# Kernel tuning notes

Hardware: AMD Instinct MI355X
Metric: run time of the kernel (lower is better)

The kernel has to match this reference:

```python
import jax, jax.numpy as jnp
import numpy as np

TEMP = 0.05
STRENGTH = 0.5

def setup_inputs() -> dict:
    key = jax.random.key(0)
    features = jax.random.normal(key, (8, 48, 48, 768), dtype=jnp.float32)
    return {"features": features}

def reference(features) -> jnp.ndarray:
    B, H, W, D = features.shape
    x = features.reshape(B, H * W, D)                      # (B, N, D)
    # L2 normalize along feature dim (eps matches torch F.normalize clamp)
    norm = jnp.maximum(jnp.linalg.norm(x, axis=-1, keepdims=True), 1e-12)
    xn = x / norm
    # cosine-similarity correlation, scaled by temperature
    corr = jnp.einsum('bnd,bmd->bnm', xn, xn) / TEMP       # (B, N, N)
    weights = jax.nn.softmax(corr, axis=-1)
    recal = jnp.einsum('bnm,bmd->bnd', weights, x)         # (B, N, D)
    enhanced = (1.0 - STRENGTH) * x + STRENGTH * recal
    return enhanced.reshape(B, H, W, D)
```

## Files before the change

### kernel.cpp

```cpp
#include <hip/hip_runtime.h>
#include <hip/hip_bf16.h>

#define B_SZ 8
#define N_SZ 2304
#define D_SZ 768
#define TEMP_INV 20.0f

typedef __attribute__((ext_vector_type(4))) float f32x4;
typedef __attribute__((ext_vector_type(8))) __bf16 bf16x8;
typedef __attribute__((ext_vector_type(8))) unsigned short u16x8;

__device__ inline void gload16(const void* g, void* l) {
  __builtin_amdgcn_global_load_lds(
      (const __attribute__((address_space(1))) unsigned int*)g,
      (__attribute__((address_space(3))) unsigned int*)l,
      16, 0, 0);
}

__device__ inline f32x4 dsr128(unsigned addr) {
  f32x4 d;
  asm volatile("ds_read_b128 %0, %1" : "=v"(d) : "v"(addr));
  return d;
}

__device__ inline float b2f(unsigned short h) {
  union { float f; unsigned u; } x;
  x.u = ((unsigned)h) << 16;
  return x.f;
}
__device__ inline unsigned short f2b(float f) {
  __hip_bfloat16 t = __float2bfloat16(f);
  return *reinterpret_cast<unsigned short*>(&t);
}

__global__ __launch_bounds__(256) void normalize_k(
    const float* __restrict__ f, __hip_bfloat16* __restrict__ xn) {
  const int row = blockIdx.x;
  const int t = threadIdx.x;
  const float* r = f + (size_t)row * D_SZ;
  float v0 = r[t], v1 = r[t + 256], v2 = r[t + 512];
  float s = v0 * v0 + v1 * v1 + v2 * v2;
#pragma unroll
  for (int m = 32; m >= 1; m >>= 1) s += __shfl_xor(s, m);
  __shared__ float red[4];
  const int wid = t >> 6, lane = t & 63;
  if (lane == 0) red[wid] = s;
  __syncthreads();
  s = red[0] + red[1] + red[2] + red[3];
  const float inv = rsqrtf(fmaxf(s, 1e-24f));
  __hip_bfloat16* o = xn + (size_t)row * D_SZ;
  o[t]       = __float2bfloat16(v0 * inv);
  o[t + 256] = __float2bfloat16(v1 * inv);
  o[t + 512] = __float2bfloat16(v2 * inv);
}

__global__ __launch_bounds__(256) void transpose_k(
    const float* __restrict__ f, __hip_bfloat16* __restrict__ xt) {
  __shared__ float tile[32][33];
  const int b = blockIdx.z;
  const int n0 = blockIdx.x * 32, d0 = blockIdx.y * 32;
  const int tx = threadIdx.x & 31, ty = threadIdx.x >> 5;
  const float* fb = f + (size_t)b * N_SZ * D_SZ;
#pragma unroll
  for (int j = 0; j < 4; ++j)
    tile[ty * 4 + j][tx] = fb[(size_t)(n0 + ty * 4 + j) * D_SZ + d0 + tx];
  __syncthreads();
  __hip_bfloat16* ob = xt + (size_t)b * D_SZ * N_SZ;
#pragma unroll
  for (int j = 0; j < 4; ++j)
    ob[(size_t)(d0 + ty * 4 + j) * N_SZ + n0 + tx] =
        __float2bfloat16(tile[tx][ty * 4 + j]);
}

__global__ __launch_bounds__(256) void softmax_k(__hip_bfloat16* corr) {
  const int t = threadIdx.x;
  const int sub = t & 31;
  const size_t row = (size_t)blockIdx.x * 8 + (t >> 5);
  unsigned short* p = (unsigned short*)(corr + row * N_SZ);
  u16x8 q[9];
  float v[72];
  float mx = -1e30f;
#pragma unroll
  for (int j = 0; j < 9; ++j) {
    q[j] = *(const u16x8*)&p[(sub + 32 * j) * 8];
#pragma unroll
    for (int e = 0; e < 8; ++e) {
      v[j * 8 + e] = b2f(q[j][e]) * TEMP_INV;
      mx = fmaxf(mx, v[j * 8 + e]);
    }
  }
#pragma unroll
  for (int m = 16; m >= 1; m >>= 1) mx = fmaxf(mx, __shfl_xor(mx, m, 32));
  float sum = 0.f;
#pragma unroll
  for (int i = 0; i < 72; ++i) {
    v[i] = __expf(v[i] - mx);
    sum += v[i];
  }
#pragma unroll
  for (int m = 16; m >= 1; m >>= 1) sum += __shfl_xor(sum, m, 32);
  const float inv = 1.0f / sum;
#pragma unroll
  for (int j = 0; j < 9; ++j) {
    u16x8 o;
#pragma unroll
    for (int e = 0; e < 8; ++e) o[e] = f2b(v[j * 8 + e] * inv);
    *(u16x8*)&p[(sub + 32 * j) * 8] = o;
  }
}

template <int MODE>
__global__ __launch_bounds__(512, 2) void gemm8_k(
    const __hip_bfloat16* __restrict__ A, const __hip_bfloat16* __restrict__ Bm,
    __hip_bfloat16* __restrict__ Cbf, const float* __restrict__ Fin,
    float* __restrict__ Fout, const int K, const int lda, const int ldb,
    const long long batchA, const long long batchB, const int ldc,
    const long long batchC, const int gx, const int gy, const int cpx) {
  __shared__ __align__(16) short lds[65536];
  const int o = blockIdx.x + gx * (blockIdx.y + gy * blockIdx.z);
  const int l = (o & 7) * cpx + (o >> 3);
  const int bx = l % gx;
  const int byz = l / gx;
  const int by = byz % gy;
  const int b = byz / gy;

  const int tid = threadIdx.x;
  const int wid = tid >> 6, lane = tid & 63;
  const int wr = wid >> 2, wc = wid & 3;
  const int fr = lane & 15, fk = lane >> 4;

  const short* Ab = (const short*)A + (size_t)b * batchA + (size_t)bx * 256 * lda;
  const short* Bb = (const short*)Bm + (size_t)b * batchB + (size_t)by * 256 * ldb;

  const int r0 = tid >> 2;
  const int gsw = ((tid & 3) ^ ((r0 >> 1) & 3)) * 8;
  const short* sa0 = Ab + (size_t)r0 * lda + gsw;
  const short* sa1 = Ab + (size_t)(r0 + 128) * lda + gsw;
  const short* sb0 = Bb + (size_t)r0 * ldb + gsw;
  const short* sb1 = Bb + (size_t)(r0 + 128) * ldb + gsw;
  const int dstT = tid * 8;

  const unsigned ldsBase = (unsigned)(unsigned long long)&lds[0];
  const int g2b = (fk ^ ((fr >> 1) & 3)) * 16;
  unsigned aOffB[8], bOffB[4];
#pragma unroll
  for (int mi = 0; mi < 8; ++mi)
    aOffB[mi] = (unsigned)((wr * 128 + mi * 16 + fr) * 64 + g2b);
#pragma unroll
  for (int ni = 0; ni < 4; ++ni)
    bOffB[ni] = (unsigned)(16384 + (wc * 64 + ni * 16 + fr) * 64 + g2b);

  f32x4 acc[8][4];
#pragma unroll
  for (int i = 0; i < 8; ++i)
#pragma unroll
    for (int j = 0; j < 4; ++j) acc[i][j] = (f32x4)0.f;

  const int T = K >> 6;
  const int UMAX = 4 * T;

  auto stage = [&](int u) {
    const int kOff = (u >> 1) * 32;
    short* d = &lds[((u >> 1) & 3) * 16384 + (u & 1) * 8192 + dstT];
    if (u & 1) {
      gload16(sb0 + kOff, d);
      gload16(sb1 + kOff, d + 4096);
    } else {
      gload16(sa0 + kOff, d);
      gload16(sa1 + kOff, d + 4096);
    }
  };

#pragma unroll
  for (int u = 0; u < 6; ++u) stage(u);
  asm volatile("s_waitcnt vmcnt(4)");
  __builtin_amdgcn_s_barrier();

  f32x4 bq[4], af[4];
  for (int t = 0; t < T; ++t) {
#pragma unroll
    for (int q = 0; q < 4; ++q) {
      const int kk = q >> 1;
      const unsigned slotB = ldsBase + (unsigned)(((2 * t + kk) & 3) * 32768);
      if ((q & 1) == 0) {
#pragma unroll
        for (int ni = 0; ni < 4; ++ni) bq[ni] = dsr128(slotB + bOffB[ni]);
      }
#pragma unroll
      for (int i = 0; i < 4; ++i)
        af[i] = dsr128(slotB + aOffB[(q & 1) * 4 + i]);
      const int u = 4 * t + q + 6;
      if (u < UMAX) stage(u);
      __builtin_amdgcn_s_barrier();
      asm volatile("s_waitcnt lgkmcnt(0)");
      __builtin_amdgcn_sched_barrier(0);
      __builtin_amdgcn_s_setprio(1);
#pragma unroll
      for (int i = 0; i < 4; ++i)
#pragma unroll
        for (int ni = 0; ni < 4; ++ni)
          acc[(q & 1) * 4 + i][ni] = __builtin_amdgcn_mfma_f32_16x16x32_bf16(
              __builtin_bit_cast(bf16x8, af[i]), __builtin_bit_cast(bf16x8, bq[ni]),
              acc[(q & 1) * 4 + i][ni], 0, 0, 0);
      __builtin_amdgcn_s_setprio(0);
      if (q == 3) {
        if (t < T - 2) {
          asm volatile("s_waitcnt vmcnt(4)");
        } else if (t == T - 2) {
          asm volatile("s_waitcnt vmcnt(0)");
        }
      }
      __builtin_amdgcn_s_barrier();
    }
  }

  const int row0 = bx * 256 + wr * 128 + fk * 4;
  const int col0 = by * 256 + wc * 64 + fr;
  if (MODE == 0) {
    __hip_bfloat16* Cb = Cbf + (size_t)b * batchC;
#pragma unroll
    for (int mi = 0; mi < 8; ++mi)
#pragma unroll
      for (int ni = 0; ni < 4; ++ni)
#pragma unroll
        for (int r = 0; r < 4; ++r)
          Cb[(size_t)(row0 + mi * 16 + r) * ldc + (col0 + ni * 16)] =
              __float2bfloat16(acc[mi][ni][r]);
  } else {
    const size_t base = (size_t)b * batchC;
#pragma unroll
    for (int mi = 0; mi < 8; ++mi)
#pragma unroll
      for (int ni = 0; ni < 4; ++ni)
#pragma unroll
        for (int r = 0; r < 4; ++r) {
          const size_t idx =
              base + (size_t)(row0 + mi * 16 + r) * ldc + (col0 + ni * 16);
          Fout[idx] = 0.5f * Fin[idx] + 0.5f * acc[mi][ni][r];
        }
  }
}

extern "C" void kernel_launch(void* const* d_in, const int* in_sizes, int n_in,
                              void* d_out, int out_size, void* d_ws,
                              size_t ws_size, hipStream_t stream) {
  const float* feat = (const float*)d_in[0];
  float* out = (float*)d_out;
  char* ws = (char*)d_ws;
  const size_t ND = (size_t)B_SZ * N_SZ * D_SZ;
  __hip_bfloat16* xn = (__hip_bfloat16*)ws;
  __hip_bfloat16* xt = (__hip_bfloat16*)(ws + ND * 2);
  __hip_bfloat16* corr = (__hip_bfloat16*)(ws + ND * 4);

  normalize_k<<<B_SZ * N_SZ, 256, 0, stream>>>(feat, xn);
  transpose_k<<<dim3(N_SZ / 32, D_SZ / 32, B_SZ), 256, 0, stream>>>(feat, xt);
  gemm8_k<0><<<dim3(9, 9, 8), 512, 0, stream>>>(
      xn, xn, corr, nullptr, nullptr, D_SZ, D_SZ, D_SZ,
      (long long)N_SZ * D_SZ, (long long)N_SZ * D_SZ, N_SZ,
      (long long)N_SZ * N_SZ, 9, 9, 81);
  softmax_k<<<B_SZ * N_SZ / 8, 256, 0, stream>>>(corr);
  gemm8_k<1><<<dim3(9, 3, 8), 512, 0, stream>>>(
      corr, xt, nullptr, feat, out, N_SZ, N_SZ, N_SZ,
      (long long)N_SZ * N_SZ, (long long)D_SZ * N_SZ, D_SZ,
      (long long)N_SZ * D_SZ, 9, 3, 27);
}
```

Before: 294.5 us.

## Double-buffer LDS fragment reads to overlap with MFMA in GEMM main loop

Restructures the GEMM inner loop so the A/B register fragments for the next sub-step are read from LDS while the MFMAs for the current sub-step run. The fragments become double-buffered in registers, one barrier per sub-step is removed, and the vmcnt wait thresholds are retuned so more global loads stay in flight. The aim is to hide LDS read latency behind matrix math. The cost is higher register pressure and more delicate wait and barrier ordering, where a mistake could cause a race.

```diff
diff --git a/kernel.cpp b/kernel.cpp
--- a/kernel.cpp
+++ b/kernel.cpp
@@ -158,6 +158,7 @@
 
   const int T = K >> 6;
   const int UMAX = 4 * T;
+  const int PMAX = 4 * T;
 
   auto stage = [&](int u) {
     const int kOff = (u >> 1) * 32;
@@ -173,44 +174,57 @@
 
 #pragma unroll
   for (int u = 0; u < 6; ++u) stage(u);
-  asm volatile("s_waitcnt vmcnt(4)");
+  asm volatile("s_waitcnt vmcnt(8)");
   __builtin_amdgcn_s_barrier();
 
-  f32x4 bq[4], af[4];
+  f32x4 af[2][4], bq[2][4];
+#pragma unroll
+  for (int ni = 0; ni < 4; ++ni) bq[0][ni] = dsr128(ldsBase + bOffB[ni]);
+#pragma unroll
+  for (int i = 0; i < 4; ++i) af[0][i] = dsr128(ldsBase + aOffB[i]);
+
   for (int t = 0; t < T; ++t) {
 #pragma unroll
     for (int q = 0; q < 4; ++q) {
-      const int kk = q >> 1;
-      const unsigned slotB = ldsBase + (unsigned)(((2 * t + kk) & 3) * 32768);
-      if ((q & 1) == 0) {
-#pragma unroll
-        for (int ni = 0; ni < 4; ++ni) bq[ni] = dsr128(slotB + bOffB[ni]);
-      }
-#pragma unroll
-      for (int i = 0; i < 4; ++i)
-        af[i] = dsr128(slotB + aOffB[(q & 1) * 4 + i]);
-      const int u = 4 * t + q + 6;
+      const int p = 4 * t + q;
+      const int u = p + 6;
       if (u < UMAX) stage(u);
-      __builtin_amdgcn_s_barrier();
       asm volatile("s_waitcnt lgkmcnt(0)");
       __builtin_amdgcn_sched_barrier(0);
-      __builtin_amdgcn_s_setprio(1);
-#pragma unroll
-      for (int i = 0; i < 4; ++i)
-#pragma unroll
-        for (int ni = 0; ni < 4; ++ni)
-          acc[(q & 1) * 4 + i][ni] = __builtin_amdgcn_mfma_f32_16x16x32_bf16(
-              __builtin_bit_cast(bf16x8, af[i]), __builtin_bit_cast(bf16x8, bq[ni]),
-              acc[(q & 1) * 4 + i][ni], 0, 0, 0);
-      __builtin_amdgcn_s_setprio(0);
-      if (q == 3) {
-        if (t < T - 2) {
+      if (q & 1) {
+        if (p <= PMAX - 7) {
+          asm volatile("s_waitcnt vmcnt(8)");
+        } else if (p == PMAX - 5) {
           asm volatile("s_waitcnt vmcnt(4)");
-        } else if (t == T - 2) {
+        } else {
           asm volatile("s_waitcnt vmcnt(0)");
         }
       }
       __builtin_amdgcn_s_barrier();
+      __builtin_amdgcn_sched_barrier(0);
+      if (p < PMAX - 1) {
+        const int hn = 2 * t + ((q + 1) >> 1);
+        const unsigned slotB = ldsBase + (unsigned)((hn & 3) * 32768);
+        if (q & 1) {
+#pragma unroll
+          for (int ni = 0; ni < 4; ++ni)
+            bq[((q + 1) >> 1) & 1][ni] = dsr128(slotB + bOffB[ni]);
+        }
+#pragma unroll
+        for (int i = 0; i < 4; ++i)
+          af[(q + 1) & 1][i] = dsr128(slotB + aOffB[((q + 1) & 1) * 4 + i]);
+      }
+      __builtin_amdgcn_sched_barrier(0);
+      __builtin_amdgcn_s_setprio(1);
+#pragma unroll
+      for (int i = 0; i < 4; ++i)
+#pragma unroll
+        for (int ni = 0; ni < 4; ++ni)
+          acc[(q & 1) * 4 + i][ni] = __builtin_amdgcn_mfma_f32_16x16x32_bf16(
+              __builtin_bit_cast(bf16x8, af[q & 1][i]),
+              __builtin_bit_cast(bf16x8, bq[(q >> 1) & 1][ni]),
+              acc[(q & 1) * 4 + i][ni], 0, 0, 0);
+      __builtin_amdgcn_s_setprio(0);
     }
   }
 
```

New measurement: 320.1 us. +8.7%, slower.

## Fuse softmax into GEMM epilogues using fixed max and atomic row sums

Applied to the files above, without the earlier changes.

Removes the separate softmax kernel. The first GEMM now writes exp(20*(s-1)) as bf16, using the fact that cosine similarity is at most 1 so the row max can be fixed, and atomically adds partial row sums into a zeroed buffer. The second GEMM scales its output by the inverse row sum in the epilogue. The main loop is also restructured to load all 8 A fragments per phase and stage two k-chunks at once, with adjusted vmcnt waits. This saves one full read/write pass over the N×N matrix, but adds float atomics and a memset, and relies on the fixed-max bound for numerical safety.

```diff
diff --git a/kernel.cpp b/kernel.cpp
--- a/kernel.cpp
+++ b/kernel.cpp
@@ -72,50 +72,14 @@
         __float2bfloat16(tile[tx][ty * 4 + j]);
 }
 
-__global__ __launch_bounds__(256) void softmax_k(__hip_bfloat16* corr) {
-  const int t = threadIdx.x;
-  const int sub = t & 31;
-  const size_t row = (size_t)blockIdx.x * 8 + (t >> 5);
-  unsigned short* p = (unsigned short*)(corr + row * N_SZ);
-  u16x8 q[9];
-  float v[72];
-  float mx = -1e30f;
-#pragma unroll
-  for (int j = 0; j < 9; ++j) {
-    q[j] = *(const u16x8*)&p[(sub + 32 * j) * 8];
-#pragma unroll
-    for (int e = 0; e < 8; ++e) {
-      v[j * 8 + e] = b2f(q[j][e]) * TEMP_INV;
-      mx = fmaxf(mx, v[j * 8 + e]);
-    }
-  }
-#pragma unroll
-  for (int m = 16; m >= 1; m >>= 1) mx = fmaxf(mx, __shfl_xor(mx, m, 32));
-  float sum = 0.f;
-#pragma unroll
-  for (int i = 0; i < 72; ++i) {
-    v[i] = __expf(v[i] - mx);
-    sum += v[i];
-  }
-#pragma unroll
-  for (int m = 16; m >= 1; m >>= 1) sum += __shfl_xor(sum, m, 32);
-  const float inv = 1.0f / sum;
-#pragma unroll
-  for (int j = 0; j < 9; ++j) {
-    u16x8 o;
-#pragma unroll
-    for (int e = 0; e < 8; ++e) o[e] = f2b(v[j * 8 + e] * inv);
-    *(u16x8*)&p[(sub + 32 * j) * 8] = o;
-  }
-}
-
 template <int MODE>
 __global__ __launch_bounds__(512, 2) void gemm8_k(
     const __hip_bfloat16* __restrict__ A, const __hip_bfloat16* __restrict__ Bm,
     __hip_bfloat16* __restrict__ Cbf, const float* __restrict__ Fin,
-    float* __restrict__ Fout, const int K, const int lda, const int ldb,
-    const long long batchA, const long long batchB, const int ldc,
-    const long long batchC, const int gx, const int gy, const int cpx) {
+    float* __restrict__ Fout, float* __restrict__ rowsum, const int K,
+    const int lda, const int ldb, const long long batchA, const long long batchB,
+    const int ldc, const long long batchC, const int gx, const int gy,
+    const int cpx) {
   __shared__ __align__(16) short lds[65536];
   const int o = blockIdx.x + gx * (blockIdx.y + gy * blockIdx.z);
   const int l = (o & 7) * cpx + (o >> 3);
@@ -157,7 +121,7 @@
     for (int j = 0; j < 4; ++j) acc[i][j] = (f32x4)0.f;
 
   const int T = K >> 6;
-  const int UMAX = 4 * T;
+  const int P = 2 * T;
 
   auto stage = [&](int u) {
     const int kOff = (u >> 1) * 32;
@@ -173,71 +137,78 @@
 
 #pragma unroll
   for (int u = 0; u < 6; ++u) stage(u);
-  asm volatile("s_waitcnt vmcnt(4)");
+  asm volatile("s_waitcnt vmcnt(8)");
   __builtin_amdgcn_s_barrier();
 
-  f32x4 bq[4], af[4];
-  for (int t = 0; t < T; ++t) {
-#pragma unroll
-    for (int q = 0; q < 4; ++q) {
-      const int kk = q >> 1;
-      const unsigned slotB = ldsBase + (unsigned)(((2 * t + kk) & 3) * 32768);
-      if ((q & 1) == 0) {
-#pragma unroll
-        for (int ni = 0; ni < 4; ++ni) bq[ni] = dsr128(slotB + bOffB[ni]);
-      }
-#pragma unroll
-      for (int i = 0; i < 4; ++i)
-        af[i] = dsr128(slotB + aOffB[(q & 1) * 4 + i]);
-      const int u = 4 * t + q + 6;
-      if (u < UMAX) stage(u);
-      __builtin_amdgcn_s_barrier();
-      asm volatile("s_waitcnt lgkmcnt(0)");
-      __builtin_amdgcn_sched_barrier(0);
-      __builtin_amdgcn_s_setprio(1);
-#pragma unroll
-      for (int i = 0; i < 4; ++i)
-#pragma unroll
-        for (int ni = 0; ni < 4; ++ni)
-          acc[(q & 1) * 4 + i][ni] = __builtin_amdgcn_mfma_f32_16x16x32_bf16(
-              __builtin_bit_cast(bf16x8, af[i]), __builtin_bit_cast(bf16x8, bq[ni]),
-              acc[(q & 1) * 4 + i][ni], 0, 0, 0);
-      __builtin_amdgcn_s_setprio(0);
-      if (q == 3) {
-        if (t < T - 2) {
-          asm volatile("s_waitcnt vmcnt(4)");
-        } else if (t == T - 2) {
-          asm volatile("s_waitcnt vmcnt(0)");
-        }
-      }
-      __builtin_amdgcn_s_barrier();
+  f32x4 af[8], bq[4];
+  for (int p = 0; p < P; ++p) {
+    const unsigned slotB = ldsBase + (unsigned)((p & 3) * 32768);
+#pragma unroll
+    for (int ni = 0; ni < 4; ++ni) bq[ni] = dsr128(slotB + bOffB[ni]);
+#pragma unroll
+    for (int i = 0; i < 8; ++i) af[i] = dsr128(slotB + aOffB[i]);
+    if (p + 3 < P) {
+      stage(2 * (p + 3));
+      stage(2 * (p + 3) + 1);
     }
+    __builtin_amdgcn_s_barrier();
+    asm volatile("s_waitcnt lgkmcnt(0)");
+    __builtin_amdgcn_sched_barrier(0);
+    __builtin_amdgcn_s_setprio(1);
+#pragma unroll
+    for (int i = 0; i < 8; ++i)
+#pragma unroll
+      for (int ni = 0; ni < 4; ++ni)
+        acc[i][ni] = __builtin_amdgcn_mfma_f32_16x16x32_bf16(
+            __builtin_bit_cast(bf16x8, af[i]), __builtin_bit_cast(bf16x8, bq[ni]),
+            acc[i][ni], 0, 0, 0);
+    __builtin_amdgcn_s_setprio(0);
+    if (p < P - 3) {
+      asm volatile("s_waitcnt vmcnt(8)");
+    } else if (p == P - 3) {
+      asm volatile("s_waitcnt vmcnt(4)");
+    } else if (p == P - 2) {
+      asm volatile("s_waitcnt vmcnt(0)");
+    }
+    __builtin_amdgcn_s_barrier();
   }
 
   const int row0 = bx * 256 + wr * 128 + fk * 4;
   const int col0 = by * 256 + wc * 64 + fr;
   if (MODE == 0) {
-    __hip_bfloat16* Cb = Cbf + (size_t)b * batchC;
+    unsigned short* Cb = (unsigned short*)(Cbf + (size_t)b * batchC);
+    float* rsb = rowsum + (size_t)b * N_SZ;
 #pragma unroll
     for (int mi = 0; mi < 8; ++mi)
 #pragma unroll
-      for (int ni = 0; ni < 4; ++ni)
-#pragma unroll
-        for (int r = 0; r < 4; ++r)
-          Cb[(size_t)(row0 + mi * 16 + r) * ldc + (col0 + ni * 16)] =
-              __float2bfloat16(acc[mi][ni][r]);
+      for (int r = 0; r < 4; ++r) {
+        float psum = 0.f;
+#pragma unroll
+        for (int ni = 0; ni < 4; ++ni) {
+          const float e = __expf(fmaf(20.f, acc[mi][ni][r], -20.f));
+          const unsigned short h = f2b(e);
+          Cb[(size_t)(row0 + mi * 16 + r) * ldc + (col0 + ni * 16)] = h;
+          psum += b2f(h);
+        }
+#pragma unroll
+        for (int m = 1; m <= 8; m <<= 1) psum += __shfl_xor(psum, m, 16);
+        if (fr == 0) atomicAdd(&rsb[row0 + mi * 16 + r], psum);
+      }
   } else {
     const size_t base = (size_t)b * batchC;
+    const float* rsb = rowsum + (size_t)b * N_SZ;
 #pragma unroll
     for (int mi = 0; mi < 8; ++mi)
 #pragma unroll
-      for (int ni = 0; ni < 4; ++ni)
-#pragma unroll
-        for (int r = 0; r < 4; ++r) {
+      for (int r = 0; r < 4; ++r) {
+        const float inv = 1.0f / rsb[row0 + mi * 16 + r];
+#pragma unroll
+        for (int ni = 0; ni < 4; ++ni) {
           const size_t idx =
               base + (size_t)(row0 + mi * 16 + r) * ldc + (col0 + ni * 16);
-          Fout[idx] = 0.5f * Fin[idx] + 0.5f * acc[mi][ni][r];
+          Fout[idx] = 0.5f * Fin[idx] + 0.5f * acc[mi][ni][r] * inv;
         }
+      }
   }
 }
 
@@ -251,16 +222,17 @@
   __hip_bfloat16* xn = (__hip_bfloat16*)ws;
   __hip_bfloat16* xt = (__hip_bfloat16*)(ws + ND * 2);
   __hip_bfloat16* corr = (__hip_bfloat16*)(ws + ND * 4);
-
+  float* rowsum = (float*)(ws + ND * 4 + (size_t)B_SZ * N_SZ * N_SZ * 2);
+
+  hipMemsetAsync(rowsum, 0, (size_t)B_SZ * N_SZ * 4, stream);
   normalize_k<<<B_SZ * N_SZ, 256, 0, stream>>>(feat, xn);
   transpose_k<<<dim3(N_SZ / 32, D_SZ / 32, B_SZ), 256, 0, stream>>>(feat, xt);
   gemm8_k<0><<<dim3(9, 9, 8), 512, 0, stream>>>(
-      xn, xn, corr, nullptr, nullptr, D_SZ, D_SZ, D_SZ,
+      xn, xn, corr, nullptr, nullptr, rowsum, D_SZ, D_SZ, D_SZ,
       (long long)N_SZ * D_SZ, (long long)N_SZ * D_SZ, N_SZ,
       (long long)N_SZ * N_SZ, 9, 9, 81);
-  softmax_k<<<B_SZ * N_SZ / 8, 256, 0, stream>>>(corr);
   gemm8_k<1><<<dim3(9, 3, 8), 512, 0, stream>>>(
-      corr, xt, nullptr, feat, out, N_SZ, N_SZ, N_SZ,
+      corr, xt, nullptr, feat, out, rowsum, N_SZ, N_SZ, N_SZ,
       (long long)N_SZ * N_SZ, (long long)D_SZ * N_SZ, D_SZ,
       (long long)N_SZ * D_SZ, 9, 3, 27);
 }
```

New measurement: 285.6 us. 1.03x faster.
